# Performance work log

Measured on AMD Instinct MI355X. Metric: run time of the kernel, lower is better.

Reference implementation:

```python
import jax, jax.numpy as jnp
import numpy as np

B, S, HID = 1, 2048, 2048
NH, NKV, HD = 16, 4, 128
ROPE_BASE = 10000.0


def _rope(q, k, positions):
    # q: [B,NH,S,HD], k: [B,NKV,S,HD]; rotate-half RoPE
    half = HD // 2
    inv_freq = 1.0 / (ROPE_BASE ** (jnp.arange(half, dtype=jnp.float32) / half))
    ang = positions.astype(jnp.float32)[:, None] * inv_freq  # [S, half]
    cos, sin = jnp.cos(ang), jnp.sin(ang)

    def apply(x):
        x1, x2 = x[..., :half], x[..., half:]
        return jnp.concatenate([x1 * cos - x2 * sin, x1 * sin + x2 * cos], axis=-1)

    return apply(q), apply(k)


def setup_inputs() -> dict:
    key = jax.random.key(0)
    ks = jax.random.split(key, 5)
    hidden_states = jax.random.normal(ks[0], (B, S, HID), dtype=jnp.float32)
    positions = jnp.arange(S, dtype=jnp.int32)
    # additive causal mask (finite large negative instead of -inf)
    mask = jnp.triu(jnp.full((S, S), -1e9, dtype=jnp.float32), k=1)[None, None]
    scale = 0.02
    Wq = jax.random.normal(ks[1], (HID, NH * HD), dtype=jnp.float32) * scale
    Wk = jax.random.normal(ks[2], (HID, NKV * HD), dtype=jnp.float32) * scale
    Wv = jax.random.normal(ks[3], (HID, NKV * HD), dtype=jnp.float32) * scale
    Wo = jax.random.normal(ks[4], (NH * HD, HID), dtype=jnp.float32) * scale
    return {"hidden_states": hidden_states, "positions": positions, "mask": mask,
            "Wq": Wq, "Wk": Wk, "Wv": Wv, "Wo": Wo}


def reference(hidden_states, positions, mask, Wq, Wk, Wv, Wo):
    groups = NH // NKV
    q = (hidden_states @ Wq).reshape(B, S, NH, HD).transpose(0, 2, 1, 3)
    k = (hidden_states @ Wk).reshape(B, S, NKV, HD).transpose(0, 2, 1, 3)
    v = (hidden_states @ Wv).reshape(B, S, NKV, HD).transpose(0, 2, 1, 3)
    q, k = _rope(q, k, positions)
    # GQA: duplicate kv heads (repeat_interleave along head dim)
    k = jnp.repeat(k, groups, axis=1)
    v = jnp.repeat(v, groups, axis=1)
    scale = 1.0 / jnp.sqrt(jnp.float32(HD))
    scores = jnp.einsum('bhqd,bhkd->bhqk', q, k) * scale + mask
    attn = jax.nn.softmax(scores.astype(jnp.float32), axis=-1).astype(q.dtype)
    out = jnp.einsum('bhqk,bhkd->bhqd', attn, v)
    out = out.transpose(0, 2, 1, 3).reshape(B, S, NH * HD)
    output = out @ Wo
    return (output, k, v)
```

## Files before the change

kernel.cpp:

```cpp
#include <hip/hip_runtime.h>
#include <hip/hip_bf16.h>
#include <math.h>

#define S_LEN 2048
#define HID_DIM 2048
#define NH 16
#define NKV 4
#define HD 128

typedef __attribute__((ext_vector_type(8))) short bf16x8;
typedef __attribute__((ext_vector_type(4))) float f32x4;

__device__ inline unsigned short f2bf(float f) {
  unsigned int u = __float_as_uint(f);
  unsigned int r = u + 0x7FFFu + ((u >> 16) & 1u);
  return (unsigned short)(r >> 16);
}
__device__ inline float bf2f(unsigned short u) {
  return __uint_as_float(((unsigned int)u) << 16);
}

__global__ __launch_bounds__(256) void f32_to_bf16_kernel(
    const float* __restrict__ x, unsigned short* __restrict__ y, int n)
{
  int i = (blockIdx.x * 256 + threadIdx.x) * 4;
  if (i < n) {
    float4 v = *(const float4*)&x[i];
    ushort4 o;
    o.x = f2bf(v.x); o.y = f2bf(v.y); o.z = f2bf(v.z); o.w = f2bf(v.w);
    *(ushort4*)&y[i] = o;
  }
}

__global__ __launch_bounds__(256) void transpose_all(
    const float* __restrict__ Wq, const float* __restrict__ Wk,
    const float* __restrict__ Wv, const float* __restrict__ Wo,
    unsigned short* __restrict__ WT, unsigned short* __restrict__ WoT)
{
  __shared__ float t[32][33];
  const int z = blockIdx.z;
  const float* W; unsigned short* D; int N;
  if (z == 0)      { W = Wq; D = WT;                          N = 2048; }
  else if (z == 1) { W = Wk; D = WT + (size_t)2048 * 2048;    N = 512;  }
  else if (z == 2) { W = Wv; D = WT + (size_t)2560 * 2048;    N = 512;  }
  else             { W = Wo; D = WoT;                         N = 2048; }
  int bx = blockIdx.x * 32;
  if (bx >= N) return;
  int by = blockIdx.y * 32;
  int tx = threadIdx.x, ty = threadIdx.y;
  #pragma unroll
  for (int i = 0; i < 32; i += 8)
    t[ty + i][tx] = W[(size_t)(by + ty + i) * N + bx + tx];
  __syncthreads();
  #pragma unroll
  for (int i = 0; i < 32; i += 8)
    D[(size_t)(bx + ty + i) * 2048 + by + tx] = f2bf(t[tx][ty + i]);
}

#define GBK 64

__global__ __launch_bounds__(256) void gemm_bt_splitk(
    const unsigned short* __restrict__ A,
    const unsigned short* __restrict__ Bt,
    unsigned short* __restrict__ P,
    int M, int N, int KF)
{
  __shared__ __align__(16) unsigned short As[128 * GBK];
  __shared__ __align__(16) unsigned short Bs[128 * GBK];
  const int bm = blockIdx.y * 128, bn = blockIdx.x * 128, z = blockIdx.z;
  const int Kh = KF >> 1, k0z = z * Kh;
  const int tid = threadIdx.x, lane = tid & 63, wave = tid >> 6;
  const int wm = wave >> 1, wn = wave & 1;
  const int quad = lane >> 4, lcol = lane & 15;

  f32x4 zero = {0.f, 0.f, 0.f, 0.f};
  f32x4 acc[4][4];
  #pragma unroll
  for (int i = 0; i < 4; i++)
    #pragma unroll
    for (int j = 0; j < 4; j++) acc[i][j] = zero;

  for (int k0 = k0z; k0 < k0z + Kh; k0 += GBK) {
    #pragma unroll
    for (int i = 0; i < 4; i++) {
      int s = wave * 256 + i * 64 + lane;
      int row = s >> 3, g = (s & 7) ^ (row & 7);
      __builtin_amdgcn_global_load_lds(
          (const __attribute__((address_space(1))) void*)(A + (size_t)(bm + row) * KF + k0 + g * 8),
          (__attribute__((address_space(3))) void*)(As + (size_t)(wave * 256 + i * 64) * 8),
          16, 0, 0);
      __builtin_amdgcn_global_load_lds(
          (const __attribute__((address_space(1))) void*)(Bt + (size_t)(bn + row) * KF + k0 + g * 8),
          (__attribute__((address_space(3))) void*)(Bs + (size_t)(wave * 256 + i * 64) * 8),
          16, 0, 0);
    }
    __syncthreads();
    #pragma unroll
    for (int st = 0; st < 2; st++) {
      bf16x8 af[4], bfv[4];
      int sw = (st * 4 + quad) ^ (lcol & 7);
      #pragma unroll
      for (int mb = 0; mb < 4; mb++)
        af[mb] = *(const bf16x8*)&As[(wm * 64 + mb * 16 + lcol) * GBK + sw * 8];
      #pragma unroll
      for (int nb = 0; nb < 4; nb++)
        bfv[nb] = *(const bf16x8*)&Bs[(wn * 64 + nb * 16 + lcol) * GBK + sw * 8];
      #pragma unroll
      for (int mb = 0; mb < 4; mb++)
        #pragma unroll
        for (int nb = 0; nb < 4; nb++)
          acc[mb][nb] = __builtin_amdgcn_mfma_f32_16x16x32_bf16(af[mb], bfv[nb], acc[mb][nb], 0, 0, 0);
    }
    __syncthreads();
  }
  unsigned short* Pz = P + (size_t)z * M * N;
  #pragma unroll
  for (int mb = 0; mb < 4; mb++)
    #pragma unroll
    for (int nb = 0; nb < 4; nb++)
      #pragma unroll
      for (int r = 0; r < 4; r++) {
        int mm = bm + wm * 64 + mb * 16 + quad * 4 + r;
        int nn = bn + wn * 64 + nb * 16 + lcol;
        Pz[(size_t)mm * N + nn] = f2bf(acc[mb][nb][r]);
      }
}

__global__ __launch_bounds__(256) void add_out_kernel(
    const unsigned short* __restrict__ P0, const unsigned short* __restrict__ P1,
    float* __restrict__ out, int n)
{
  int i = (blockIdx.x * 256 + threadIdx.x) * 8;
  if (i < n) {
    uint4 a = *(const uint4*)&P0[i];
    uint4 b = *(const uint4*)&P1[i];
    float4 o0, o1;
    o0.x = __uint_as_float(a.x << 16) + __uint_as_float(b.x << 16);
    o0.y = __uint_as_float(a.x & 0xFFFF0000u) + __uint_as_float(b.x & 0xFFFF0000u);
    o0.z = __uint_as_float(a.y << 16) + __uint_as_float(b.y << 16);
    o0.w = __uint_as_float(a.y & 0xFFFF0000u) + __uint_as_float(b.y & 0xFFFF0000u);
    o1.x = __uint_as_float(a.z << 16) + __uint_as_float(b.z << 16);
    o1.y = __uint_as_float(a.z & 0xFFFF0000u) + __uint_as_float(b.z & 0xFFFF0000u);
    o1.z = __uint_as_float(a.w << 16) + __uint_as_float(b.w << 16);
    o1.w = __uint_as_float(a.w & 0xFFFF0000u) + __uint_as_float(b.w & 0xFFFF0000u);
    *(float4*)&out[i] = o0;
    *(float4*)&out[i + 4] = o1;
  }
}

__global__ __launch_bounds__(256) void rope_prepv_kernel(
    const unsigned short* __restrict__ P0,
    const unsigned short* __restrict__ P1,
    const int* __restrict__ positions,
    unsigned short* __restrict__ q_ws,
    unsigned short* __restrict__ k_ws,
    float* __restrict__ outk,
    float* __restrict__ outv,
    unsigned short* __restrict__ vT)
{
  __shared__ float t[32][33];
  if (blockIdx.x < 2048) {
    const float QSCALE = 0.08838834764831845f * 1.4426950408889634f;
    int s = blockIdx.x;
    float pos = (float)positions[s];
    const unsigned short* r0 = &P0[(size_t)s * 3072];
    const unsigned short* r1 = &P1[(size_t)s * 3072];
    int tt = threadIdx.x;
    int j = tt & 63, grp = tt >> 6;
    float freq = expf(-(float)j * 0.14391156831212787f);
    float ang = pos * freq;
    float sn, c;
    sincosf(ang, &sn, &c);
    #pragma unroll
    for (int ci = 0; ci < 5; ci++) {
      int ch = grp * 5 + ci;
      if (ch < NH) {
        int i1 = ch * HD + j, i2 = i1 + 64;
        float x1 = bf2f(r0[i1]) + bf2f(r1[i1]);
        float x2 = bf2f(r0[i2]) + bf2f(r1[i2]);
        float o1 = x1 * c - x2 * sn;
        float o2 = x1 * sn + x2 * c;
        size_t base = ((size_t)ch * S_LEN + s) * HD;
        q_ws[base + j] = f2bf(o1 * QSCALE);
        q_ws[base + j + 64] = f2bf(o2 * QSCALE);
      } else {
        int kv = ch - NH;
        int i1 = 2048 + kv * HD + j, i2 = i1 + 64;
        float x1 = bf2f(r0[i1]) + bf2f(r1[i1]);
        float x2 = bf2f(r0[i2]) + bf2f(r1[i2]);
        float o1 = x1 * c - x2 * sn;
        float o2 = x1 * sn + x2 * c;
        size_t kbase = ((size_t)kv * S_LEN + s) * HD;
        k_ws[kbase + j] = f2bf(o1);
        k_ws[kbase + j + 64] = f2bf(o2);
        #pragma unroll
        for (int g = 0; g < 4; g++) {
          size_t ob = ((size_t)(kv * 4 + g) * S_LEN + s) * HD;
          outk[ob + j] = o1;
          outk[ob + j + 64] = o2;
        }
      }
    }
  } else {
    int b = blockIdx.x - 2048;
    int s0 = (b & 63) * 32, d0 = ((b >> 6) & 3) * 32, kv = b >> 8;
    int tx = threadIdx.x & 31, ty = threadIdx.x >> 5;
    #pragma unroll
    for (int i = 0; i < 32; i += 8) {
      size_t idx = (size_t)(s0 + ty + i) * 3072 + 2560 + kv * HD + d0 + tx;
      t[ty + i][tx] = bf2f(P0[idx]) + bf2f(P1[idx]);
    }
    __syncthreads();
    #pragma unroll
    for (int i = 0; i < 32; i += 8) {
      float val = t[ty + i][tx];
      #pragma unroll
      for (int g = 0; g < 4; g++)
        outv[((size_t)(kv * 4 + g) * S_LEN + s0 + ty + i) * HD + d0 + tx] = val;
    }
    #pragma unroll
    for (int i = 0; i < 32; i += 8)
      vT[((size_t)kv * HD + d0 + ty + i) * S_LEN + s0 + tx] = f2bf(t[tx][ty + i]);
  }
}

__device__ inline void stage_k_tile(const unsigned short* kbase, unsigned short* dst,
                                    int wave, int lane) {
  #pragma unroll
  for (int i = 0; i < 4; i++) {
    int row = wave * 16 + i * 4 + (lane >> 4);
    int c = (lane & 15) ^ (row & 7);
    __builtin_amdgcn_global_load_lds(
        (const __attribute__((address_space(1))) void*)(kbase + (size_t)row * HD + c * 8),
        (__attribute__((address_space(3))) void*)(dst + (wave * 16 + i * 4) * 128),
        16, 0, 0);
  }
}

__device__ inline void stage_v_tile(const unsigned short* vbase, unsigned short* dst,
                                    int wave, int lane) {
  #pragma unroll
  for (int i = 0; i < 4; i++) {
    int row = wave * 32 + i * 8 + (lane >> 3);
    int c = (lane & 7) ^ (row & 7);
    __builtin_amdgcn_global_load_lds(
        (const __attribute__((address_space(1))) void*)(vbase + (size_t)row * S_LEN + c * 8),
        (__attribute__((address_space(3))) void*)(dst + (wave * 32 + i * 8) * 64),
        16, 0, 0);
  }
}

#define PLD 72
#define C2F 23.082320654223414f

__global__ __launch_bounds__(256) void flash_attn3(
    const unsigned short* __restrict__ q_ws,
    const unsigned short* __restrict__ k_ws,
    const unsigned short* __restrict__ vT_ws,
    unsigned short* __restrict__ attn_ws)
{
  __shared__ __align__(16) unsigned short Ks[2][64 * 128];
  __shared__ __align__(16) unsigned short Vs[128 * 64];
  __shared__ __align__(16) unsigned short Ps[4][16 * PLD];
  const int b = blockIdx.x;
  const int u = b >> 4, h = b & 15, kvh = h >> 2;
  const int qt = (u < 16) ? (31 - u) : (u - 16);
  const int tid = threadIdx.x, lane = tid & 63, wave = tid >> 6;
  const int quad = lane >> 4, lcol = lane & 15;
  const int qrow = qt * 64 + wave * 16 + lcol;

  const unsigned short* kh = k_ws + (size_t)kvh * S_LEN * HD;
  const unsigned short* vh = vT_ws + (size_t)kvh * HD * S_LEN;

  bf16x8 qf[4];
  {
    const unsigned short* qp = &q_ws[((size_t)h * S_LEN + qrow) * HD + quad * 8];
    #pragma unroll
    for (int st = 0; st < 4; st++) qf[st] = *(const bf16x8*)&qp[st * 32];
  }
  f32x4 zero = {0.f, 0.f, 0.f, 0.f};
  f32x4 o_acc[8];
  #pragma unroll
  for (int i = 0; i < 8; i++) o_acc[i] = zero;
  float l_acc = 0.f;

  stage_k_tile(kh, &Ks[0][0], wave, lane);

  for (int kt = 0; kt <= qt; kt++) {
    int cur = kt & 1;
    __syncthreads();
    stage_v_tile(vh + kt * 64, &Vs[0], wave, lane);
    if (kt < qt) stage_k_tile(kh + (size_t)(kt + 1) * 64 * HD, &Ks[cur ^ 1][0], wave, lane);

    f32x4 sc[4];
    #pragma unroll
    for (int kb = 0; kb < 4; kb++) {
      sc[kb] = zero;
      #pragma unroll
      for (int st = 0; st < 4; st++) {
        int krow = kb * 16 + lcol;
        bf16x8 kf = *(const bf16x8*)&Ks[cur][krow * 128 + (((st * 4 + quad) ^ (lcol & 7)) * 8)];
        sc[kb] = __builtin_amdgcn_mfma_f32_16x16x32_bf16(kf, qf[st], sc[kb], 0, 0, 0);
      }
    }

    float pv[4][4];
    if (kt < qt) {
      #pragma unroll
      for (int kb = 0; kb < 4; kb++)
        #pragma unroll
        for (int r = 0; r < 4; r++) {
          float p = exp2f(sc[kb][r] - C2F);
          pv[kb][r] = p;
          l_acc += p;
        }
    } else {
      #pragma unroll
      for (int kb = 0; kb < 4; kb++)
        #pragma unroll
        for (int r = 0; r < 4; r++) {
          int key = kt * 64 + kb * 16 + quad * 4 + r;
          float p = (key <= qrow) ? exp2f(sc[kb][r] - C2F) : 0.f;
          pv[kb][r] = p;
          l_acc += p;
        }
    }

    unsigned short* myPs = &Ps[wave][0];
    #pragma unroll
    for (int kb = 0; kb < 4; kb++) {
      unsigned int u0 = (__float_as_uint(pv[kb][0]) + 0x8000u) >> 16;
      unsigned int u1 = (__float_as_uint(pv[kb][1]) + 0x8000u) & 0xFFFF0000u;
      unsigned int u2 = (__float_as_uint(pv[kb][2]) + 0x8000u) >> 16;
      unsigned int u3 = (__float_as_uint(pv[kb][3]) + 0x8000u) & 0xFFFF0000u;
      uint2 w2; w2.x = u0 | u1; w2.y = u2 | u3;
      *(uint2*)&myPs[lcol * PLD + kb * 16 + quad * 4] = w2;
    }
    __syncthreads();

    bf16x8 pa0 = *(const bf16x8*)&myPs[lcol * PLD + quad * 8];
    bf16x8 pa1 = *(const bf16x8*)&myPs[lcol * PLD + 32 + quad * 8];
    #pragma unroll
    for (int ob = 0; ob < 8; ob++) {
      int vrow = ob * 16 + lcol, sw = lcol & 7;
      bf16x8 v0 = *(const bf16x8*)&Vs[vrow * 64 + ((quad ^ sw) * 8)];
      bf16x8 v1 = *(const bf16x8*)&Vs[vrow * 64 + (((quad + 4) ^ sw) * 8)];
      o_acc[ob] = __builtin_amdgcn_mfma_f32_16x16x32_bf16(pa0, v0, o_acc[ob], 0, 0, 0);
      o_acc[ob] = __builtin_amdgcn_mfma_f32_16x16x32_bf16(pa1, v1, o_acc[ob], 0, 0, 0);
    }
  }

  float l = l_acc;
  l += __shfl_xor(l, 16);
  l += __shfl_xor(l, 32);
  float l_t[4];
  #pragma unroll
  for (int r = 0; r < 4; r++)
    l_t[r] = __shfl(l, (lane & 48) + quad * 4 + r);
  #pragma unroll
  for (int r = 0; r < 4; r++) {
    float inv = 1.f / l_t[r];
    int row = qt * 64 + wave * 16 + quad * 4 + r;
    #pragma unroll
    for (int ob = 0; ob < 8; ob++)
      attn_ws[(size_t)row * (NH * HD) + h * HD + ob * 16 + lcol] = f2bf(o_acc[ob][r] * inv);
  }
}

extern "C" void kernel_launch(void* const* d_in, const int* in_sizes, int n_in,
                              void* d_out, int out_size, void* d_ws, size_t ws_size,
                              hipStream_t stream)
{
  const float* hidden    = (const float*)d_in[0];
  const int*   positions = (const int*)d_in[1];
  const float* Wq = (const float*)d_in[3];
  const float* Wk = (const float*)d_in[4];
  const float* Wv = (const float*)d_in[5];
  const float* Wo = (const float*)d_in[6];

  float* out  = (float*)d_out;
  float* outk = out + (size_t)S_LEN * HID_DIM;
  float* outv = outk + (size_t)NH * S_LEN * HD;

  char* ws = (char*)d_ws;
  unsigned short* h_bf   = (unsigned short*)(ws);
  unsigned short* WT     = (unsigned short*)(ws + ((size_t)8  << 20));
  unsigned short* WoT    = (unsigned short*)(ws + ((size_t)20 << 20));
  unsigned short* qkvP   = (unsigned short*)(ws + ((size_t)28 << 20));
  unsigned short* q_ws   = (unsigned short*)(ws + ((size_t)52 << 20));
  unsigned short* k_ws   = (unsigned short*)(ws + ((size_t)60 << 20));
  unsigned short* vT_ws  = (unsigned short*)(ws + ((size_t)62 << 20));
  unsigned short* attn   = (unsigned short*)(ws + ((size_t)64 << 20));
  unsigned short* outP   = qkvP;
  unsigned short* qkvP1  = qkvP + (size_t)S_LEN * 3072;
  unsigned short* outP1  = outP + (size_t)S_LEN * HID_DIM;

  f32_to_bf16_kernel<<<4096, 256, 0, stream>>>(hidden, h_bf, S_LEN * HID_DIM);
  transpose_all<<<dim3(64, 64, 4), dim3(32, 8), 0, stream>>>(Wq, Wk, Wv, Wo, WT, WoT);

  gemm_bt_splitk<<<dim3(24, 16, 2), 256, 0, stream>>>(h_bf, WT, qkvP, 2048, 3072, 2048);

  rope_prepv_kernel<<<3072, 256, 0, stream>>>(qkvP, qkvP1, positions,
                                              q_ws, k_ws, outk, outv, vT_ws);

  flash_attn3<<<dim3(512), 256, 0, stream>>>(q_ws, k_ws, vT_ws, attn);

  gemm_bt_splitk<<<dim3(16, 16, 2), 256, 0, stream>>>(attn, WoT, outP, 2048, 2048, 2048);
  add_out_kernel<<<2048, 256, 0, stream>>>(outP, outP1, out, S_LEN * HID_DIM);
}
```

Before: 248.0 us.

## Replace split-K GEMM with 256x256-tile double-buffered phased pipelined GEMM

The 128x128 split-K bf16 GEMM used for the QKV and output projections is replaced by a 512-thread kernel with 256x256 tiles. Each K step is split into 32-wide halves held in double-buffered dynamic LDS (128 KB), and the MFMA sub-phases are interleaved with async global-to-LDS prefetch, explicit vmcnt waits, barriers and s_setprio. The aim is more data reuse per block and global-load latency hidden behind MFMA work. In exchange the grid shrinks a lot (192 and 128 blocks), which may leave many CUs idle, and the large LDS request limits occupancy to one block per CU.

```diff
diff --git a/kernel.cpp b/kernel.cpp
--- a/kernel.cpp
+++ b/kernel.cpp
@@ -10,6 +10,9 @@
 
 typedef __attribute__((ext_vector_type(8))) short bf16x8;
 typedef __attribute__((ext_vector_type(4))) float f32x4;
+
+#define AS1 __attribute__((address_space(1)))
+#define AS3 __attribute__((address_space(3)))
 
 __device__ inline unsigned short f2bf(float f) {
   unsigned int u = __float_as_uint(f);
@@ -57,72 +60,136 @@
     D[(size_t)(bx + ty + i) * 2048 + by + tx] = f2bf(t[tx][ty + i]);
 }
 
-#define GBK 64
-
-__global__ __launch_bounds__(256) void gemm_bt_splitk(
+__global__ __launch_bounds__(512) void gemm_bt_8phase(
     const unsigned short* __restrict__ A,
     const unsigned short* __restrict__ Bt,
     unsigned short* __restrict__ P,
     int M, int N, int KF)
 {
-  __shared__ __align__(16) unsigned short As[128 * GBK];
-  __shared__ __align__(16) unsigned short Bs[128 * GBK];
-  const int bm = blockIdx.y * 128, bn = blockIdx.x * 128, z = blockIdx.z;
+  extern __shared__ unsigned short smem[];
+  unsigned short* Ab = smem;
+  unsigned short* Bb = smem + 32768;
+  const int bm = blockIdx.y * 256, bn = blockIdx.x * 256, z = blockIdx.z;
   const int Kh = KF >> 1, k0z = z * Kh;
+  const int NT = Kh >> 6;
   const int tid = threadIdx.x, lane = tid & 63, wave = tid >> 6;
-  const int wm = wave >> 1, wn = wave & 1;
+  const int wm = wave >> 2, wn = wave & 3;
   const int quad = lane >> 4, lcol = lane & 15;
 
+  auto stageA = [&](int t, int kh) {
+    const unsigned short* src = A + (size_t)bm * KF + k0z + t * 64 + kh * 32;
+    unsigned short* dst = Ab + (((t & 1) * 2 + kh) << 13);
+    #pragma unroll
+    for (int i = 0; i < 2; i++) {
+      int s = i * 512 + tid;
+      int row = s >> 2, dc = s & 3, g = dc ^ ((row >> 1) & 3);
+      __builtin_amdgcn_global_load_lds(
+          (const AS1 void*)(src + (size_t)row * KF + g * 8),
+          (AS3 void*)(dst + s * 8), 16, 0, 0);
+    }
+  };
+  auto stageB = [&](int t, int kh) {
+    const unsigned short* src = Bt + (size_t)bn * KF + k0z + t * 64 + kh * 32;
+    unsigned short* dst = Bb + (((t & 1) * 2 + kh) << 13);
+    #pragma unroll
+    for (int i = 0; i < 2; i++) {
+      int s = i * 512 + tid;
+      int row = s >> 2, dc = s & 3, g = dc ^ ((row >> 1) & 3);
+      __builtin_amdgcn_global_load_lds(
+          (const AS1 void*)(src + (size_t)row * KF + g * 8),
+          (AS3 void*)(dst + s * 8), 16, 0, 0);
+    }
+  };
+  auto ldA = [&](int cur, int kh, int mh, bf16x8* af) {
+    const unsigned short* base = Ab + ((cur * 2 + kh) << 13);
+    #pragma unroll
+    for (int m = 0; m < 4; m++) {
+      int row = wm * 128 + (mh * 4 + m) * 16 + lcol;
+      int ch = quad ^ ((row >> 1) & 3);
+      af[m] = *(const bf16x8*)&base[row * 32 + ch * 8];
+    }
+  };
+  auto ldB = [&](int cur, int kh, bf16x8* bfr) {
+    const unsigned short* base = Bb + ((cur * 2 + kh) << 13);
+    #pragma unroll
+    for (int n = 0; n < 4; n++) {
+      int row = wn * 64 + n * 16 + lcol;
+      int ch = quad ^ ((row >> 1) & 3);
+      bfr[n] = *(const bf16x8*)&base[row * 32 + ch * 8];
+    }
+  };
+
   f32x4 zero = {0.f, 0.f, 0.f, 0.f};
-  f32x4 acc[4][4];
-  #pragma unroll
-  for (int i = 0; i < 4; i++)
+  f32x4 acc[8][4];
+  #pragma unroll
+  for (int i = 0; i < 8; i++)
     #pragma unroll
     for (int j = 0; j < 4; j++) acc[i][j] = zero;
 
-  for (int k0 = k0z; k0 < k0z + Kh; k0 += GBK) {
-    #pragma unroll
-    for (int i = 0; i < 4; i++) {
-      int s = wave * 256 + i * 64 + lane;
-      int row = s >> 3, g = (s & 7) ^ (row & 7);
-      __builtin_amdgcn_global_load_lds(
-          (const __attribute__((address_space(1))) void*)(A + (size_t)(bm + row) * KF + k0 + g * 8),
-          (__attribute__((address_space(3))) void*)(As + (size_t)(wave * 256 + i * 64) * 8),
-          16, 0, 0);
-      __builtin_amdgcn_global_load_lds(
-          (const __attribute__((address_space(1))) void*)(Bt + (size_t)(bn + row) * KF + k0 + g * 8),
-          (__attribute__((address_space(3))) void*)(Bs + (size_t)(wave * 256 + i * 64) * 8),
-          16, 0, 0);
-    }
-    __syncthreads();
-    #pragma unroll
-    for (int st = 0; st < 2; st++) {
-      bf16x8 af[4], bfv[4];
-      int sw = (st * 4 + quad) ^ (lcol & 7);
-      #pragma unroll
-      for (int mb = 0; mb < 4; mb++)
-        af[mb] = *(const bf16x8*)&As[(wm * 64 + mb * 16 + lcol) * GBK + sw * 8];
-      #pragma unroll
-      for (int nb = 0; nb < 4; nb++)
-        bfv[nb] = *(const bf16x8*)&Bs[(wn * 64 + nb * 16 + lcol) * GBK + sw * 8];
-      #pragma unroll
-      for (int mb = 0; mb < 4; mb++)
-        #pragma unroll
-        for (int nb = 0; nb < 4; nb++)
-          acc[mb][nb] = __builtin_amdgcn_mfma_f32_16x16x32_bf16(af[mb], bfv[nb], acc[mb][nb], 0, 0, 0);
-    }
-    __syncthreads();
-  }
+  stageA(0, 0); stageB(0, 0); stageA(0, 1); stageB(0, 1);
+  if (NT > 1) { stageA(1, 0); stageB(1, 0); }
+  asm volatile("s_waitcnt vmcnt(8)" ::: "memory");
+  __builtin_amdgcn_s_barrier();
+
+  for (int t = 0; t < NT; t++) {
+    const int cur = t & 1;
+    bf16x8 af[4], bfr[4];
+    ldB(cur, 0, bfr);
+    ldA(cur, 0, 0, af);
+    __builtin_amdgcn_s_barrier();
+    if (t + 1 < NT) stageA(t + 1, 1);
+    __builtin_amdgcn_s_setprio(1);
+    #pragma unroll
+    for (int m = 0; m < 4; m++)
+      #pragma unroll
+      for (int n = 0; n < 4; n++)
+        acc[m][n] = __builtin_amdgcn_mfma_f32_16x16x32_bf16(af[m], bfr[n], acc[m][n], 0, 0, 0);
+    __builtin_amdgcn_s_setprio(0);
+    ldA(cur, 0, 1, af);
+    asm volatile("s_waitcnt vmcnt(6)" ::: "memory");
+    __builtin_amdgcn_s_barrier();
+    if (t + 1 < NT) stageB(t + 1, 1);
+    __builtin_amdgcn_s_setprio(1);
+    #pragma unroll
+    for (int m = 0; m < 4; m++)
+      #pragma unroll
+      for (int n = 0; n < 4; n++)
+        acc[4 + m][n] = __builtin_amdgcn_mfma_f32_16x16x32_bf16(af[m], bfr[n], acc[4 + m][n], 0, 0, 0);
+    __builtin_amdgcn_s_setprio(0);
+    ldB(cur, 1, bfr);
+    ldA(cur, 1, 0, af);
+    __builtin_amdgcn_s_barrier();
+    if (t + 2 < NT) stageA(t + 2, 0);
+    __builtin_amdgcn_s_setprio(1);
+    #pragma unroll
+    for (int m = 0; m < 4; m++)
+      #pragma unroll
+      for (int n = 0; n < 4; n++)
+        acc[m][n] = __builtin_amdgcn_mfma_f32_16x16x32_bf16(af[m], bfr[n], acc[m][n], 0, 0, 0);
+    __builtin_amdgcn_s_setprio(0);
+    ldA(cur, 1, 1, af);
+    asm volatile("s_waitcnt vmcnt(6)" ::: "memory");
+    __builtin_amdgcn_s_barrier();
+    if (t + 2 < NT) stageB(t + 2, 0);
+    __builtin_amdgcn_s_setprio(1);
+    #pragma unroll
+    for (int m = 0; m < 4; m++)
+      #pragma unroll
+      for (int n = 0; n < 4; n++)
+        acc[4 + m][n] = __builtin_amdgcn_mfma_f32_16x16x32_bf16(af[m], bfr[n], acc[4 + m][n], 0, 0, 0);
+    __builtin_amdgcn_s_setprio(0);
+  }
+
   unsigned short* Pz = P + (size_t)z * M * N;
   #pragma unroll
-  for (int mb = 0; mb < 4; mb++)
-    #pragma unroll
-    for (int nb = 0; nb < 4; nb++)
+  for (int mr = 0; mr < 8; mr++)
+    #pragma unroll
+    for (int nr = 0; nr < 4; nr++)
       #pragma unroll
       for (int r = 0; r < 4; r++) {
-        int mm = bm + wm * 64 + mb * 16 + quad * 4 + r;
-        int nn = bn + wn * 64 + nb * 16 + lcol;
-        Pz[(size_t)mm * N + nn] = f2bf(acc[mb][nb][r]);
+        int mm = bm + wm * 128 + mr * 16 + quad * 4 + r;
+        int nn = bn + wn * 64 + nr * 16 + lcol;
+        Pz[(size_t)mm * N + nn] = f2bf(acc[mr][nr][r]);
       }
 }
 
@@ -231,8 +298,8 @@
     int row = wave * 16 + i * 4 + (lane >> 4);
     int c = (lane & 15) ^ (row & 7);
     __builtin_amdgcn_global_load_lds(
-        (const __attribute__((address_space(1))) void*)(kbase + (size_t)row * HD + c * 8),
-        (__attribute__((address_space(3))) void*)(dst + (wave * 16 + i * 4) * 128),
+        (const AS1 void*)(kbase + (size_t)row * HD + c * 8),
+        (AS3 void*)(dst + (wave * 16 + i * 4) * 128),
         16, 0, 0);
   }
 }
@@ -244,8 +311,8 @@
     int row = wave * 32 + i * 8 + (lane >> 3);
     int c = (lane & 7) ^ (row & 7);
     __builtin_amdgcn_global_load_lds(
-        (const __attribute__((address_space(1))) void*)(vbase + (size_t)row * S_LEN + c * 8),
-        (__attribute__((address_space(3))) void*)(dst + (wave * 32 + i * 8) * 64),
+        (const AS1 void*)(vbase + (size_t)row * S_LEN + c * 8),
+        (AS3 void*)(dst + (wave * 32 + i * 8) * 64),
         16, 0, 0);
   }
 }
@@ -398,13 +465,13 @@
   f32_to_bf16_kernel<<<4096, 256, 0, stream>>>(hidden, h_bf, S_LEN * HID_DIM);
   transpose_all<<<dim3(64, 64, 4), dim3(32, 8), 0, stream>>>(Wq, Wk, Wv, Wo, WT, WoT);
 
-  gemm_bt_splitk<<<dim3(24, 16, 2), 256, 0, stream>>>(h_bf, WT, qkvP, 2048, 3072, 2048);
+  gemm_bt_8phase<<<dim3(12, 8, 2), 512, 131072, stream>>>(h_bf, WT, qkvP, 2048, 3072, 2048);
 
   rope_prepv_kernel<<<3072, 256, 0, stream>>>(qkvP, qkvP1, positions,
                                               q_ws, k_ws, outk, outv, vT_ws);
 
   flash_attn3<<<dim3(512), 256, 0, stream>>>(q_ws, k_ws, vT_ws, attn);
 
-  gemm_bt_splitk<<<dim3(16, 16, 2), 256, 0, stream>>>(attn, WoT, outP, 2048, 2048, 2048);
+  gemm_bt_8phase<<<dim3(8, 8, 2), 512, 131072, stream>>>(attn, WoT, outP, 2048, 2048, 2048);
   add_out_kernel<<<2048, 256, 0, stream>>>(outP, outP1, out, S_LEN * HID_DIM);
 }
```

Measured after the change: 247.4 us. About the same (-0.2%).
